# Optimization experiments

Measured on AMD Instinct MI355X. Metric: run time of the kernel, lower is better.

Reference implementation:

```python
import jax, jax.numpy as jnp
import numpy as np

B, L, W, K, G = 8, 2048, 1024, 5, 2
OFFSET_SCALE = 2.0
EPS = 1e-5


def setup_inputs() -> dict:
    key = jax.random.key(0)
    ks = jax.random.split(key, 6)
    x = jax.random.normal(ks[0], (B, L, W), jnp.float32)
    # True = padded position
    lengths = jax.random.randint(ks[1], (B,), L // 2, L + 1)
    mask = jnp.arange(L)[None, :] >= lengths[:, None]
    # offset predictor (pointwise): one fractional offset per kernel tap
    w_off = jax.random.normal(ks[2], (W, K), jnp.float32) * 0.02
    b_off = jnp.zeros((K,), jnp.float32)
    # grouped conv weights: [groups, out_per_group, in_per_group, K]
    conv_w = jax.random.normal(ks[3], (G, W // G, W // G, K), jnp.float32) * 0.02
    conv_b = jnp.zeros((W,), jnp.float32)
    gamma = jnp.ones((W,), jnp.float32)
    beta = jnp.zeros((W,), jnp.float32)
    proj_w = jax.random.normal(ks[4], (W,), jnp.float32) * 0.02
    proj_b = jnp.zeros((), jnp.float32)
    return dict(x=x, mask=mask, w_off=w_off, b_off=b_off, conv_w=conv_w,
                conv_b=conv_b, gamma=gamma, beta=beta, proj_w=proj_w, proj_b=proj_b)


def _deform_conv1d(x, w_off, b_off, conv_w, conv_b):
    # x: [B, L, W]; returns [B, L, W]
    Bb, Ll, Ww = x.shape
    Gg, Co, Ci, Kk = conv_w.shape
    # per-position, per-tap fractional offsets in [-offset_scale, offset_scale]
    offsets = jnp.tanh(x @ w_off + b_off) * OFFSET_SCALE            # [B, L, K]
    taps = jnp.arange(Kk, dtype=x.dtype) - (Kk - 1) / 2.0           # centered taps
    pos = jnp.arange(Ll, dtype=x.dtype)[None, :, None] + taps[None, None, :] + offsets  # [B,L,K]
    p0 = jnp.floor(pos)
    frac = pos - p0                                                  # [B, L, K]
    p0i = p0.astype(jnp.int32)
    bidx = jnp.arange(Bb)[:, None, None]

    def gather(idx):
        valid = (idx >= 0) & (idx < Ll)                              # zero padding outside
        samp = x[bidx, jnp.clip(idx, 0, Ll - 1)]                     # [B, L, K, W]
        return samp * valid[..., None].astype(x.dtype)

    # linear interpolation between floor and floor+1 samples
    samp = gather(p0i) * (1.0 - frac)[..., None] + gather(p0i + 1) * frac[..., None]
    samp = samp.reshape(Bb, Ll, Kk, Gg, Ci)                          # split channels into groups
    out = jnp.einsum('blkgc,gock->blgo', samp, conv_w).reshape(Bb, Ll, Gg * Co)
    return out + conv_b


def reference(x, mask, w_off, b_off, conv_w, conv_b, gamma, beta, proj_w, proj_b):
    h = _deform_conv1d(x, w_off, b_off, conv_w, conv_b)              # [B, L, W]
    # LayerNorm over width
    mu = jnp.mean(h, axis=-1, keepdims=True)
    var = jnp.mean((h - mu) ** 2, axis=-1, keepdims=True)
    h = (h - mu) * jax.lax.rsqrt(var + EPS) * gamma + beta
    # dropout is identity in eval mode
    h = jnp.where(mask[..., None], 0.0, h)                           # masked fill
    lengths = jnp.maximum(jnp.sum(~mask, axis=1, keepdims=True).astype(h.dtype), 1.0)
    pooled = jnp.sum(h, axis=1) / lengths                            # [B, W]
    return pooled @ proj_w + proj_b                                  # [B]
```

## Files before the change

kernel.cpp:

```cpp
#include <hip/hip_runtime.h>
#include <hip/hip_bf16.h>

constexpr int Bb = 8, Ll = 2048, Ww = 1024;
constexpr int BL = Bb * Ll;

typedef short bf16x8 __attribute__((ext_vector_type(8)));
typedef float f32x4  __attribute__((ext_vector_type(4)));

__device__ inline unsigned short f2bf(float f) {
    union { float f; unsigned u; } v; v.f = f;
    unsigned u = v.u;
    unsigned r = (u + 0x7fffu + ((u >> 16) & 1u)) >> 16;
    return (unsigned short)r;
}
__device__ inline unsigned lerp_pair(unsigned pa, unsigned pb, float w0, float w1) {
    union { unsigned u; float f; } alo, ahi, blo, bhi;
    alo.u = pa << 16;  ahi.u = pa & 0xffff0000u;
    blo.u = pb << 16;  bhi.u = pb & 0xffff0000u;
    float hlo = w0 * alo.f + w1 * blo.f;
    float hhi = w0 * ahi.f + w1 * bhi.f;
    union { __hip_bfloat162 h2; unsigned u; } r;
    r.h2 = __float22bfloat162_rn(float2{hlo, hhi});
    return r.u;
}

__device__ inline void gl_lds16(const unsigned short* g, unsigned short* l) {
    __builtin_amdgcn_global_load_lds(
        (const __attribute__((address_space(1))) unsigned int*)g,
        (__attribute__((address_space(3))) unsigned int*)l, 16, 0, 0);
}

__global__ __launch_bounds__(256) void prep_kernel(
    const float* __restrict__ x, const float* __restrict__ w_off, const float* __restrict__ b_off,
    const float* __restrict__ conv_w, const void* __restrict__ mraw,
    unsigned short* __restrict__ x_bf, float4* __restrict__ pk,
    unsigned short* __restrict__ w_t, float* __restrict__ maskf)
{
    const int blk = blockIdx.x;
    const int tid = threadIdx.x;
    __shared__ float wt[5][1024];

    if (blk < 4096) {
        #pragma unroll
        for (int r = 0; r < 5; ++r) {
            const int f4 = tid + 256 * r;
            float4 v = *(const float4*)&w_off[f4 * 4];
            const int idx = f4 * 4;
            const float* ve = (const float*)&v;
            #pragma unroll
            for (int e = 0; e < 4; ++e) {
                const int li = idx + e;
                wt[li % 5][li / 5] = ve[e];
            }
        }

        const int wave = tid >> 6, lane = tid & 63;
        const int bl = blk * 4 + wave;
        const int l = bl & (Ll - 1);
        const int c0 = lane * 16;

        const float* xr = x + (size_t)bl * Ww + c0;
        float4 v0 = *(const float4*)(xr + 0);
        float4 v1 = *(const float4*)(xr + 4);
        float4 v2 = *(const float4*)(xr + 8);
        float4 v3 = *(const float4*)(xr + 12);
        float xv[16] = { v0.x,v0.y,v0.z,v0.w, v1.x,v1.y,v1.z,v1.w,
                         v2.x,v2.y,v2.z,v2.w, v3.x,v3.y,v3.z,v3.w };

        uint4 pa, pb;
        unsigned* pu = (unsigned*)&pa;
        #pragma unroll
        for (int j = 0; j < 4; j++) pu[j] = (unsigned)f2bf(xv[j*2]) | ((unsigned)f2bf(xv[j*2+1]) << 16);
        pu = (unsigned*)&pb;
        #pragma unroll
        for (int j = 0; j < 4; j++) pu[j] = (unsigned)f2bf(xv[8+j*2]) | ((unsigned)f2bf(xv[8+j*2+1]) << 16);
        *(uint4*)&x_bf[(size_t)bl * Ww + c0]     = pa;
        *(uint4*)&x_bf[(size_t)bl * Ww + c0 + 8] = pb;

        float xs[16];
        const float* xrow = x + (size_t)bl * Ww;
        #pragma unroll
        for (int jj = 0; jj < 16; jj++) xs[jj] = xrow[lane + 64 * jj];

        __syncthreads();

        float acc[5] = {0.f, 0.f, 0.f, 0.f, 0.f};
        #pragma unroll
        for (int jj = 0; jj < 16; jj++) {
            const int c = lane + 64 * jj;
            #pragma unroll
            for (int k = 0; k < 5; k++) acc[k] += xs[jj] * wt[k][c];
        }
        #pragma unroll
        for (int k = 0; k < 5; k++)
            #pragma unroll
            for (int off = 32; off; off >>= 1) acc[k] += __shfl_xor(acc[k], off);

        if (lane < 5) {
            float s = (lane == 0) ? acc[0] : (lane == 1) ? acc[1] : (lane == 2) ? acc[2]
                    : (lane == 3) ? acc[3] : acc[4];
            s += b_off[lane];
            float offv = tanhf(s) * 2.0f;
            float pos = (float)l + (float)(lane - 2) + offv;
            float p0 = floorf(pos);
            float frac = pos - p0;
            int i0 = (int)p0;
            int i1 = i0 + 1;
            int ok0 = (i0 >= 0) && (i0 < Ll);
            int ok1 = (i1 >= 0) && (i1 < Ll);
            float4 pkv;
            pkv.x = __int_as_float(min(max(i0, 0), Ll - 1));
            pkv.y = __int_as_float(min(max(i1, 0), Ll - 1));
            pkv.z = ok0 ? (1.0f - frac) : 0.0f;
            pkv.w = ok1 ? frac : 0.0f;
            pk[bl * 5 + lane] = pkv;
        }
    } else if (blk < 4352) {
        int t = (blk - 4096) * 256 + tid;
        int oct = t & 63;
        int o   = (t >> 6) & 511;
        int g   = t >> 15;
        const float* src = conv_w + ((size_t)(g * 512 + o) * 512 + oct * 8) * 5;
        float f[40];
        #pragma unroll
        for (int j = 0; j < 10; j++) *(float4*)&f[j * 4] = *(const float4*)&src[j * 4];
        int r = o & 127, ob = o >> 7, cs = oct >> 2, q = oct & 3;
        int base16 = ((g * 20 + ob) * 16 + cs) * 512 + r * 4 + (q ^ (r & 3));
        #pragma unroll
        for (int k = 0; k < 5; k++) {
            ushort4 lo, hi;
            lo.x = f2bf(f[0 * 5 + k]); lo.y = f2bf(f[1 * 5 + k]);
            lo.z = f2bf(f[2 * 5 + k]); lo.w = f2bf(f[3 * 5 + k]);
            hi.x = f2bf(f[4 * 5 + k]); hi.y = f2bf(f[5 * 5 + k]);
            hi.z = f2bf(f[6 * 5 + k]); hi.w = f2bf(f[7 * 5 + k]);
            int dst16 = base16 + k * 4 * 16 * 512;
            *(ushort4*)&w_t[(size_t)dst16 * 8]     = lo;
            *(ushort4*)&w_t[(size_t)dst16 * 8 + 4] = hi;
        }
    } else {
        const unsigned char* mb = (const unsigned char*)mraw;
        const unsigned* mw = (const unsigned*)mraw;
        int nonint = 0, notf = 0, hasf = 0;
        for (int i = tid; i < BL; i += 256) { if ((i & 3) && mb[i]) nonint = 1; }
        for (int i = tid; i < BL / 4; i += 256) {
            unsigned w = mw[i];
            if (w == 0x3f800000u) hasf = 1; else if (w) notf = 1;
        }
        __shared__ int sf[3];
        if (tid == 0) { sf[0] = 0; sf[1] = 0; sf[2] = 0; }
        __syncthreads();
        if (nonint) atomicOr(&sf[0], 1);
        if (notf)   atomicOr(&sf[1], 1);
        if (hasf)   atomicOr(&sf[2], 1);
        __syncthreads();
        const int is_f32  = (!sf[1]) && sf[2];
        const int is_bool = (!is_f32) && sf[0];
        const int gid = (blk - 4352) * 256 + tid;
        for (int i = gid; i < BL; i += 4096) {
            int masked = is_bool ? (mb[i] != 0) : (mw[i] != 0u);
            maskf[i] = masked ? 0.0f : 1.0f;
        }
    }
}

__global__ __launch_bounds__(256, 2) void gemm_kernel(
    const unsigned short* __restrict__ x_bf, const unsigned short* __restrict__ w_t,
    const float4* __restrict__ pk, const float* __restrict__ conv_b,
    unsigned short* __restrict__ h)
{
    __shared__ unsigned short Bs[2][2 * 4096];
    __shared__ unsigned short As[2][4096];
    const int tid = threadIdx.x;
    const int mt = blockIdx.x;
    const int nhalf = blockIdx.y;
    const int g = blockIdx.z;
    const int b = mt >> 4;
    const int lane = tid & 63, wave = tid >> 6;
    const int wr4 = (wave >> 1) * 4;
    const int imgsel = wave & 1;
    const int l15 = lane & 15, l4 = lane >> 4;
    const int sw = (l4 ^ (l15 & 3)) * 8;

    const int arow = ((tid >> 6) << 4) + (tid & 15);
    const int oct8 = ((tid >> 4) & 3) * 8;
    const int bl_a = mt * 128 + arow;
    const int bl_b = bl_a + 64;
    const int gbase = g * 512;

    unsigned off0a, off1a, off0b, off1b;
    float w0a, w1a, w0b, w1b;
    auto load_meta = [&](int k2) {
        float4 pa = pk[bl_a * 5 + k2];
        float4 pb = pk[bl_b * 5 + k2];
        off0a = (unsigned)(((b << 11) + __float_as_int(pa.x)) * Ww + gbase);
        off1a = (unsigned)(((b << 11) + __float_as_int(pa.y)) * Ww + gbase);
        w0a = pa.z; w1a = pa.w;
        off0b = (unsigned)(((b << 11) + __float_as_int(pb.x)) * Ww + gbase);
        off1b = (unsigned)(((b << 11) + __float_as_int(pb.y)) * Ww + gbase);
        w0b = pb.z; w1b = pb.w;
    };
    auto build_A = [&](int cs2, unsigned short* dst) {
        const int ch = cs2 * 32 + oct8;
        uint4 ua = *(const uint4*)(x_bf + off0a + ch);
        uint4 ub = *(const uint4*)(x_bf + off1a + ch);
        uint4 uc = *(const uint4*)(x_bf + off0b + ch);
        uint4 ud = *(const uint4*)(x_bf + off1b + ch);
        uint4 ra, rb;
        ra.x = lerp_pair(ua.x, ub.x, w0a, w1a);
        ra.y = lerp_pair(ua.y, ub.y, w0a, w1a);
        ra.z = lerp_pair(ua.z, ub.z, w0a, w1a);
        ra.w = lerp_pair(ua.w, ub.w, w0a, w1a);
        rb.x = lerp_pair(uc.x, ud.x, w0b, w1b);
        rb.y = lerp_pair(uc.y, ud.y, w0b, w1b);
        rb.z = lerp_pair(uc.z, ud.z, w0b, w1b);
        rb.w = lerp_pair(uc.w, ud.w, w0b, w1b);
        *(uint4*)&dst[tid * 8]         = ra;
        *(uint4*)&dst[(tid + 256) * 8] = rb;
    };

    {
        const int nt0 = nhalf * 2;
        const unsigned short* W0 = w_t + ((size_t)((g * 20 + nt0) * 16 + 0)) * 4096;
        const unsigned short* W1 = w_t + ((size_t)((g * 20 + nt0 + 1) * 16 + 0)) * 4096;
        gl_lds16(W0 + tid * 8,        &Bs[0][tid * 8]);
        gl_lds16(W0 + 2048 + tid * 8, &Bs[0][2048 + tid * 8]);
        gl_lds16(W1 + tid * 8,        &Bs[0][4096 + tid * 8]);
        gl_lds16(W1 + 2048 + tid * 8, &Bs[0][4096 + 2048 + tid * 8]);
    }
    load_meta(0);
    build_A(0, &As[0][0]);
    __syncthreads();

    f32x4 acc[4][8];
    #pragma unroll
    for (int i = 0; i < 4; i++)
        #pragma unroll
        for (int j = 0; j < 8; j++) acc[i][j] = (f32x4){0.f, 0.f, 0.f, 0.f};

    int buf = 0;
    for (int it = 0; it < 80; ++it) {
        const int it2 = it + 1;
        if (it2 < 80) {
            const int k2 = it2 >> 4, cs2 = it2 & 15;
            const int nt0 = k2 * 4 + nhalf * 2;
            const unsigned short* W0 = w_t + ((size_t)((g * 20 + nt0) * 16 + cs2)) * 4096;
            const unsigned short* W1 = w_t + ((size_t)((g * 20 + nt0 + 1) * 16 + cs2)) * 4096;
            unsigned short* bd = &Bs[buf ^ 1][0];
            gl_lds16(W0 + tid * 8,        bd + tid * 8);
            gl_lds16(W0 + 2048 + tid * 8, bd + 2048 + tid * 8);
            gl_lds16(W1 + tid * 8,        bd + 4096 + tid * 8);
            gl_lds16(W1 + 2048 + tid * 8, bd + 4096 + 2048 + tid * 8);
            if (cs2 == 0) load_meta(k2);
            build_A(cs2, &As[buf ^ 1][0]);
        }
        {
            bf16x8 af[4];
            #pragma unroll
            for (int i = 0; i < 4; i++)
                af[i] = *(const bf16x8*)&As[buf][((wr4 + i) * 64 + lane) * 8];
            const unsigned short* bsrc = &Bs[buf][imgsel * 4096];
            #pragma unroll
            for (int j = 0; j < 8; j++) {
                bf16x8 bj = *(const bf16x8*)&bsrc[(j * 16 + l15) * 32 + sw];
                #pragma unroll
                for (int i = 0; i < 4; i++)
                    acc[i][j] = __builtin_amdgcn_mfma_f32_16x16x32_bf16(af[i], bj, acc[i][j], 0, 0, 0);
            }
        }
        __syncthreads();
        buf ^= 1;
    }

    #pragma unroll
    for (int j = 0; j < 8; j++) {
        const int col = g * 512 + nhalf * 256 + imgsel * 128 + j * 16 + l15;
        const float bias = conv_b[col];
        #pragma unroll
        for (int i = 0; i < 4; i++) {
            const int row0 = mt * 128 + (wave >> 1) * 64 + i * 16 + l4 * 4;
            #pragma unroll
            for (int rr = 0; rr < 4; rr++)
                h[(size_t)(row0 + rr) * Ww + col] = f2bf(acc[i][j][rr] + bias);
        }
    }
}

__global__ __launch_bounds__(256) void lnpool_kernel(
    const unsigned short* __restrict__ h, const float* __restrict__ gamma,
    const float* __restrict__ maskf, float* __restrict__ partial)
{
    const int tid = threadIdx.x;
    const int wave = tid >> 6, lane = tid & 63;
    const int c0 = lane * 16;
    const int bl0 = blockIdx.x * 16 + wave * 4;

    float g16[16];
    #pragma unroll
    for (int j = 0; j < 4; j++) {
        float4 gv = *(const float4*)(gamma + c0 + j * 4);
        g16[j*4+0] = gv.x; g16[j*4+1] = gv.y; g16[j*4+2] = gv.z; g16[j*4+3] = gv.w;
    }
    float pacc[16];
    #pragma unroll
    for (int j = 0; j < 16; j++) pacc[j] = 0.f;

    #pragma unroll
    for (int r = 0; r < 4; r++) {
        const int bl = bl0 + r;
        const float m = maskf[bl];
        const uint4 ha = *(const uint4*)(h + (size_t)bl * Ww + c0);
        const uint4 hb = *(const uint4*)(h + (size_t)bl * Ww + c0 + 8);
        float hf[16];
        const unsigned* pw = (const unsigned*)&ha;
        #pragma unroll
        for (int j = 0; j < 4; j++) {
            union { unsigned u; float f; } lo, hi;
            lo.u = pw[j] << 16; hi.u = pw[j] & 0xffff0000u;
            hf[j*2] = lo.f; hf[j*2+1] = hi.f;
        }
        pw = (const unsigned*)&hb;
        #pragma unroll
        for (int j = 0; j < 4; j++) {
            union { unsigned u; float f; } lo, hi;
            lo.u = pw[j] << 16; hi.u = pw[j] & 0xffff0000u;
            hf[8+j*2] = lo.f; hf[8+j*2+1] = hi.f;
        }
        float s1 = 0.f, s2 = 0.f;
        #pragma unroll
        for (int j = 0; j < 16; j++) { s1 += hf[j]; s2 += hf[j] * hf[j]; }
        #pragma unroll
        for (int off = 32; off; off >>= 1) {
            s1 += __shfl_xor(s1, off);
            s2 += __shfl_xor(s2, off);
        }
        const float mu = s1 * (1.0f / 1024.0f);
        const float var = s2 * (1.0f / 1024.0f) - mu * mu;
        const float rstd = rsqrtf(var + 1e-5f) * m;
        #pragma unroll
        for (int j = 0; j < 16; j++) pacc[j] += (hf[j] - mu) * rstd * g16[j];
    }
    __shared__ float spool[4][1024];
    #pragma unroll
    for (int j = 0; j < 4; j++)
        *(float4*)&spool[wave][c0 + j * 4] = *(float4*)&pacc[j * 4];
    __syncthreads();
    const int ch = tid * 4;
    float4 a = *(float4*)&spool[0][ch];
    float4 bq = *(float4*)&spool[1][ch];
    float4 cq = *(float4*)&spool[2][ch];
    float4 dq = *(float4*)&spool[3][ch];
    float4 s; s.x = a.x + bq.x + cq.x + dq.x; s.y = a.y + bq.y + cq.y + dq.y;
    s.z = a.z + bq.z + cq.z + dq.z; s.w = a.w + bq.w + cq.w + dq.w;
    *(float4*)&partial[(size_t)blockIdx.x * 1024 + ch] = s;
}

__global__ void final_kernel(const float* __restrict__ partial, const float* __restrict__ maskf,
                             const float* __restrict__ beta, const float* __restrict__ proj_w,
                             const float* __restrict__ proj_b, float* __restrict__ out)
{
    int b = blockIdx.x;
    int tid = threadIdx.x;
    float len = 0.f;
    for (int l = tid; l < Ll; l += 256) len += maskf[b * Ll + l];
    const int ch = tid * 4;
    float4 ps = {0.f, 0.f, 0.f, 0.f};
    #pragma unroll 8
    for (int j = 0; j < 128; ++j) {
        float4 v = *(const float4*)&partial[(size_t)((b << 7) + j) * 1024 + ch];
        ps.x += v.x; ps.y += v.y; ps.z += v.z; ps.w += v.w;
    }
    float4 pw = *(const float4*)&proj_w[ch];
    float4 bt = *(const float4*)&beta[ch];
    float dotP = ps.x * pw.x + ps.y * pw.y + ps.z * pw.z + ps.w * pw.w;
    float dotB = bt.x * pw.x + bt.y * pw.y + bt.z * pw.z + bt.w * pw.w;
    for (int off = 32; off; off >>= 1) {
        len  += __shfl_down(len, off);
        dotP += __shfl_down(dotP, off);
        dotB += __shfl_down(dotB, off);
    }
    __shared__ float rl[4], rp[4], rb[4];
    int wave = tid >> 6, lane = tid & 63;
    if (lane == 0) { rl[wave] = len; rp[wave] = dotP; rb[wave] = dotB; }
    __syncthreads();
    if (tid == 0) {
        float Lt = rl[0] + rl[1] + rl[2] + rl[3];
        float Pt = rp[0] + rp[1] + rp[2] + rp[3];
        float Bt = rb[0] + rb[1] + rb[2] + rb[3];
        out[b] = Pt / fmaxf(Lt, 1.0f) + Bt + proj_b[0];
    }
}


extern "C" void kernel_launch(void* const* d_in, const int* in_sizes, int n_in,
                              void* d_out, int out_size, void* d_ws, size_t ws_size,
                              hipStream_t stream)
{
    const float* x      = (const float*)d_in[0];
    const void*  mask   = d_in[1];
    const float* w_off  = (const float*)d_in[2];
    const float* b_off  = (const float*)d_in[3];
    const float* conv_w = (const float*)d_in[4];
    const float* conv_b = (const float*)d_in[5];
    const float* gamma  = (const float*)d_in[6];
    const float* beta   = (const float*)d_in[7];
    const float* proj_w = (const float*)d_in[8];
    const float* proj_b = (const float*)d_in[9];
    float* out = (float*)d_out;

    char* ws = (char*)d_ws;
    float* maskf         = (float*)(ws + 0);
    float4* pk           = (float4*)(ws + 98320);
    unsigned short* w_t  = (unsigned short*)(ws + 1409040);
    unsigned short* x_bf = (unsigned short*)(ws + 6651920);
    float* partial       = (float*)(ws + 6651920);
    unsigned short* h    = (unsigned short*)(ws + 40206352);

    prep_kernel<<<4368, 256, 0, stream>>>(x, w_off, b_off, conv_w, mask,
                                          x_bf, pk, w_t, maskf);
    gemm_kernel<<<dim3(128, 2, 2), 256, 0, stream>>>(x_bf, w_t, pk, conv_b, h);
    lnpool_kernel<<<1024, 256, 0, stream>>>(h, gamma, maskf, partial);
    final_kernel<<<8, 256, 0, stream>>>(partial, maskf, beta, proj_w, proj_b, out);
}
```

Baseline: 292.8 us.

## Change LDS swizzle, raise GEMM occupancy hint, widen final reduction block

The XOR swizzle for the weight tile in LDS now keys on (row>>1)&3 instead of row&3, in both the prep writer and the GEMM reader, to change the bank-conflict pattern of the MFMA operand loads. The GEMM launch bound rises from 2 to 3 waves-per-EU blocks, which caps register use and may cause spills. The final reduction kernel runs 1024 threads per batch, splitting the 128 partial rows across four thread groups so each thread serially adds fewer rows.

```diff
diff --git a/kernel.cpp b/kernel.cpp
--- a/kernel.cpp
+++ b/kernel.cpp
@@ -125,7 +125,7 @@
         #pragma unroll
         for (int j = 0; j < 10; j++) *(float4*)&f[j * 4] = *(const float4*)&src[j * 4];
         int r = o & 127, ob = o >> 7, cs = oct >> 2, q = oct & 3;
-        int base16 = ((g * 20 + ob) * 16 + cs) * 512 + r * 4 + (q ^ (r & 3));
+        int base16 = ((g * 20 + ob) * 16 + cs) * 512 + r * 4 + (q ^ ((r >> 1) & 3));
         #pragma unroll
         for (int k = 0; k < 5; k++) {
             ushort4 lo, hi;
@@ -163,7 +163,7 @@
     }
 }
 
-__global__ __launch_bounds__(256, 2) void gemm_kernel(
+__global__ __launch_bounds__(256, 3) void gemm_kernel(
     const unsigned short* __restrict__ x_bf, const unsigned short* __restrict__ w_t,
     const float4* __restrict__ pk, const float* __restrict__ conv_b,
     unsigned short* __restrict__ h)
@@ -179,7 +179,7 @@
     const int wr4 = (wave >> 1) * 4;
     const int imgsel = wave & 1;
     const int l15 = lane & 15, l4 = lane >> 4;
-    const int sw = (l4 ^ (l15 & 3)) * 8;
+    const int sw = (l4 ^ ((l15 >> 1) & 3)) * 8;
 
     const int arow = ((tid >> 6) << 4) + (tid & 15);
     const int oct8 = ((tid >> 4) & 3) * 8;
@@ -354,38 +354,43 @@
     *(float4*)&partial[(size_t)blockIdx.x * 1024 + ch] = s;
 }
 
-__global__ void final_kernel(const float* __restrict__ partial, const float* __restrict__ maskf,
-                             const float* __restrict__ beta, const float* __restrict__ proj_w,
-                             const float* __restrict__ proj_b, float* __restrict__ out)
+__global__ __launch_bounds__(1024) void final_kernel(
+    const float* __restrict__ partial, const float* __restrict__ maskf,
+    const float* __restrict__ beta, const float* __restrict__ proj_w,
+    const float* __restrict__ proj_b, float* __restrict__ out)
 {
-    int b = blockIdx.x;
-    int tid = threadIdx.x;
-    float len = 0.f;
-    for (int l = tid; l < Ll; l += 256) len += maskf[b * Ll + l];
-    const int ch = tid * 4;
+    const int b = blockIdx.x;
+    const int tid = threadIdx.x;
+    const int rc = tid >> 8;
+    const int ch = (tid & 255) * 4;
+
     float4 ps = {0.f, 0.f, 0.f, 0.f};
-    #pragma unroll 8
-    for (int j = 0; j < 128; ++j) {
+    #pragma unroll 4
+    for (int j = rc * 32; j < rc * 32 + 32; ++j) {
         float4 v = *(const float4*)&partial[(size_t)((b << 7) + j) * 1024 + ch];
         ps.x += v.x; ps.y += v.y; ps.z += v.z; ps.w += v.w;
     }
+    float len = maskf[b * Ll + tid] + maskf[b * Ll + 1024 + tid];
     float4 pw = *(const float4*)&proj_w[ch];
-    float4 bt = *(const float4*)&beta[ch];
     float dotP = ps.x * pw.x + ps.y * pw.y + ps.z * pw.z + ps.w * pw.w;
-    float dotB = bt.x * pw.x + bt.y * pw.y + bt.z * pw.z + bt.w * pw.w;
+    float dotB = 0.f;
+    if (rc == 0) {
+        float4 bt = *(const float4*)&beta[ch];
+        dotB = bt.x * pw.x + bt.y * pw.y + bt.z * pw.z + bt.w * pw.w;
+    }
     for (int off = 32; off; off >>= 1) {
         len  += __shfl_down(len, off);
         dotP += __shfl_down(dotP, off);
         dotB += __shfl_down(dotB, off);
     }
-    __shared__ float rl[4], rp[4], rb[4];
-    int wave = tid >> 6, lane = tid & 63;
-    if (lane == 0) { rl[wave] = len; rp[wave] = dotP; rb[wave] = dotB; }
+    __shared__ float rl[16], rp[16], rb2[16];
+    const int wave = tid >> 6, lane = tid & 63;
+    if (lane == 0) { rl[wave] = len; rp[wave] = dotP; rb2[wave] = dotB; }
     __syncthreads();
     if (tid == 0) {
-        float Lt = rl[0] + rl[1] + rl[2] + rl[3];
-        float Pt = rp[0] + rp[1] + rp[2] + rp[3];
-        float Bt = rb[0] + rb[1] + rb[2] + rb[3];
+        float Lt = 0.f, Pt = 0.f, Bt = 0.f;
+        #pragma unroll
+        for (int wv = 0; wv < 16; ++wv) { Lt += rl[wv]; Pt += rp[wv]; Bt += rb2[wv]; }
         out[b] = Pt / fmaxf(Lt, 1.0f) + Bt + proj_b[0];
     }
 }
@@ -419,5 +424,5 @@
                                           x_bf, pk, w_t, maskf);
     gemm_kernel<<<dim3(128, 2, 2), 256, 0, stream>>>(x_bf, w_t, pk, conv_b, h);
     lnpool_kernel<<<1024, 256, 0, stream>>>(h, gamma, maskf, partial);
-    final_kernel<<<8, 256, 0, stream>>>(partial, maskf, beta, proj_w, proj_b, out);
-}
+    final_kernel<<<8, 1024, 0, stream>>>(partial, maskf, beta, proj_w, proj_b, out);
+}
```

New measurement: 321.4 us. 1.1x slower.
